# Optimization experiments

Hardware: AMD Instinct MI355X
Metric: run time of the kernel (lower is better)

## Reference

```python
import jax, jax.numpy as jnp
import numpy as np

N = 50000      # num nodes
DIN = 256
DOUT = 256
E = 400000     # edges per sign
NEG_SLOPE = 0.2  # LeakyReLU(0.2)


def setup_inputs() -> dict:
    key = jax.random.key(0)
    ks = jax.random.split(key, 12)
    p = lambda k, shp: jax.random.normal(k, shp, jnp.float32) * 0.05
    return {
        "node_reps": jax.random.normal(ks[0], (N, DIN), jnp.float32),
        "adj_pos": jax.random.randint(ks[1], (2, E), 0, N, dtype=jnp.int32),
        "adj_neg": jax.random.randint(ks[2], (2, E), 0, N, dtype=jnp.int32),
        "basis": p(ks[3], (2, DIN, DOUT)),        # num_bases=num_relations=2
        "att": p(ks[4], (2, 2)),
        "mapping_func": p(ks[5], (1, 2 * DOUT)),
        "bias": p(ks[6], (1, DOUT)),
        "theta1": p(ks[7], (DOUT, DOUT)),          # HGNN_conv 1 linear weight
        "b1": jnp.zeros((DOUT,), jnp.float32),
        "theta2": p(ks[8], (DOUT, DOUT)),          # HGNN_conv 2 linear weight
        "b2": jnp.zeros((DOUT,), jnp.float32),
    }


def reference(node_reps, adj_pos, adj_neg, basis, att, mapping_func, bias,
              theta1, b1, theta2, b2):
    # basis-decomposed relation weights: Wr[r] = sum_b att[r,b] * basis[b]
    Wr = (att @ basis.reshape(2, -1)).reshape(2, DIN, DOUT)
    h_pos = node_reps @ Wr[0]
    h_neg = node_reps @ Wr[1]
    # HGNN_conv feature transforms (linear + bias)
    h_pos = h_pos @ theta1 + b1
    h_neg = h_neg @ theta2 + b2

    # edge attention score: mapping_func . concat(h[src], h[dst])
    w_src = mapping_func[0, :DOUT]
    w_dst = mapping_func[0, DOUT:]
    e_pos = h_pos[adj_pos[0]] @ w_src + h_pos[adj_pos[1]] @ w_dst  # [E]
    e_neg = h_neg[adj_neg[0]] @ w_src + h_neg[adj_neg[1]] @ w_dst  # [E]
    e_all = jnp.concatenate([e_pos, e_neg])                         # [2E]
    coeff = jax.nn.sigmoid(jnp.where(e_all > 0, e_all, NEG_SLOPE * e_all))

    # symmetric degree normalization over the union graph
    rows_all = jnp.concatenate([adj_pos[0], adj_neg[0]])
    cols_all = jnp.concatenate([adj_pos[1], adj_neg[1]])
    deg = jnp.sqrt(jax.ops.segment_sum(
        jnp.ones_like(coeff), rows_all, num_segments=N))            # [N]
    coeff = coeff / (deg[rows_all] * deg[cols_all])

    # sparse aggregation (SpecialSpmm): out[r] += coeff_e * h[c]
    h_agg_pos = jax.ops.segment_sum(
        coeff[:E, None] * h_pos[adj_pos[1]], adj_pos[0], num_segments=N)
    h_agg_neg = jax.ops.segment_sum(
        coeff[E:, None] * h_neg[adj_neg[1]], adj_neg[0], num_segments=N)

    output = h_agg_pos - h_agg_neg + bias
    return (output, h_agg_pos, h_agg_neg)
```

## Files before the change

kernel.cpp:

```cpp
#include <hip/hip_runtime.h>

#define N_NODES 50000
#define NEDGE   400000
#define SB      512
#define NSB     ((N_NODES + SB - 1) / SB)

typedef __bf16 bf16x8 __attribute__((ext_vector_type(8)));
typedef float  f32x4  __attribute__((ext_vector_type(4)));
typedef unsigned short u16x8 __attribute__((ext_vector_type(8)));

#define GLDS16(gp, lp) \
  __builtin_amdgcn_global_load_lds((const __attribute__((address_space(1))) void*)(gp), \
                                   (__attribute__((address_space(3))) void*)(lp), 16, 0, 0)

static __device__ __forceinline__ unsigned short f2bf(float f) {
  unsigned u = __float_as_uint(f);
  unsigned r = (u + 0x7fffu + ((u >> 16) & 1u)) >> 16;
  return (unsigned short)r;
}
static __device__ __forceinline__ float bf2f(unsigned short v) {
  return __uint_as_float((unsigned)v << 16);
}

__global__ void prep_kernel(const float* __restrict__ basis, const float* __restrict__ att,
                            const float* __restrict__ theta1, const float* __restrict__ theta2,
                            const float* __restrict__ bias1, const float* __restrict__ bias2,
                            unsigned short* __restrict__ Wt, float* __restrict__ biasvec) {
  const int bid = blockIdx.x;
  const int r = bid >> 8, k = bid & 255;
  const int n = threadIdx.x;
  const float a0 = att[r * 2 + 0], a1 = att[r * 2 + 1];
  const float* th = (r == 0) ? theta1 : theta2;
  float acc = 0.f;
  for (int j = 0; j < 256; ++j) {
    const float wr = a0 * basis[k * 256 + j] + a1 * basis[65536 + k * 256 + j];
    acc += wr * th[j * 256 + n];
  }
  Wt[(size_t)(r * 256 + n) * 256 + k] = f2bf(acc);
  if (k == 0) biasvec[r * 256 + n] = (r == 0) ? bias1[n] : bias2[n];
}

__global__ void cast_kernel(const float* __restrict__ in, unsigned short* __restrict__ out) {
  const long total = (long)N_NODES * 256 / 4;
  long idx = (long)blockIdx.x * blockDim.x + threadIdx.x;
  const long stride = (long)gridDim.x * blockDim.x;
  for (; idx < total; idx += stride) {
    const f32x4 v = __builtin_nontemporal_load(&((const f32x4*)in)[idx]);
    ushort4 o;
    o.x = f2bf(v.x); o.y = f2bf(v.y); o.z = f2bf(v.z); o.w = f2bf(v.w);
    ((ushort4*)out)[idx] = o;
  }
}

__global__ __launch_bounds__(256) void gemm_kernel(
    const unsigned short* __restrict__ A,
    const unsigned short* __restrict__ Wt,
    const float* __restrict__ biasvec,
    const float* __restrict__ mapping,
    unsigned short* __restrict__ H,
    float* __restrict__ sdbuf) {
  __shared__ unsigned short smem[128 * 136];
  unsigned short* sA = smem;
  unsigned short* sB = smem + 8192;
  const int tid = threadIdx.x;
  const int wave = tid >> 6, lane = tid & 63;
  const int wm = wave >> 1, wn = wave & 1;
  const int m0 = blockIdx.y * 128;
  const int n0 = blockIdx.x * 128;

  f32x4 acc[4][4];
#pragma unroll
  for (int a = 0; a < 4; ++a)
#pragma unroll
    for (int b = 0; b < 4; ++b) acc[a][b] = (f32x4){0.f, 0.f, 0.f, 0.f};

  const int srow = lane >> 3;
  const int skel = ((lane & 7) ^ srow) << 3;

  for (int ks = 0; ks < 4; ++ks) {
    const int kg = ks * 64 + skel;
#pragma unroll
    for (int c = 0; c < 4; ++c) {
      const int chunk = wave * 4 + c;
      const int row = chunk * 8 + srow;
      int rowg = m0 + row;
      rowg = rowg < N_NODES ? rowg : N_NODES - 1;
      GLDS16(A + (size_t)rowg * 256 + kg, sA + chunk * 512);
      GLDS16(Wt + (size_t)(n0 + row) * 256 + kg, sB + chunk * 512);
    }
    __syncthreads();
#pragma unroll
    for (int kk = 0; kk < 2; ++kk) {
      const int kb = (kk * 32 + ((lane >> 4) << 3)) << 1;
      bf16x8 af[4], bfr[4];
#pragma unroll
      for (int m16 = 0; m16 < 4; ++m16) {
        const int row = wm * 64 + m16 * 16 + (lane & 15);
        af[m16] = *(const bf16x8*)((const char*)sA + row * 128 + (kb ^ ((row & 7) << 4)));
      }
#pragma unroll
      for (int n16 = 0; n16 < 4; ++n16) {
        const int col = wn * 64 + n16 * 16 + (lane & 15);
        bfr[n16] = *(const bf16x8*)((const char*)sB + col * 128 + (kb ^ ((col & 7) << 4)));
      }
#pragma unroll
      for (int m16 = 0; m16 < 4; ++m16)
#pragma unroll
        for (int n16 = 0; n16 < 4; ++n16)
          acc[m16][n16] = __builtin_amdgcn_mfma_f32_16x16x32_bf16(af[m16], bfr[n16], acc[m16][n16], 0, 0, 0);
    }
    __syncthreads();
  }

  const bool sgn = (n0 >= 256);
  const int nb = (sgn ? (n0 - 256) : n0) >> 7;
  const int slice = nb * 2 + wn;
  float* __restrict__ sS = sdbuf + ((size_t)((sgn ? 2 : 0) + 0) * 4 + slice) * N_NODES;
  float* __restrict__ sD = sdbuf + ((size_t)((sgn ? 2 : 0) + 1) * 4 + slice) * N_NODES;
  float bv[4], wsv[4], wdv[4];
#pragma unroll
  for (int n16 = 0; n16 < 4; ++n16) {
    const int colg = n0 + wn * 64 + n16 * 16 + (lane & 15);
    bv[n16] = biasvec[colg];
    const int cm = colg & 255;
    wsv[n16] = mapping[cm];
    wdv[n16] = mapping[256 + cm];
  }
#pragma unroll
  for (int m16 = 0; m16 < 4; ++m16) {
    const int rowb = wm * 64 + m16 * 16 + ((lane >> 4) << 2);
#pragma unroll
    for (int j = 0; j < 4; ++j) {
      const int rowl = rowb + j;
      float vs = 0.f, vd = 0.f;
#pragma unroll
      for (int n16 = 0; n16 < 4; ++n16) {
        const float v = acc[m16][n16][j] + bv[n16];
        const int coll = wn * 64 + n16 * 16 + (lane & 15);
        smem[rowl * 136 + coll] = f2bf(v);
        vs += v * wsv[n16];
        vd += v * wdv[n16];
      }
#pragma unroll
      for (int off = 1; off < 16; off <<= 1) { vs += __shfl_xor(vs, off); vd += __shfl_xor(vd, off); }
      const int rowg = m0 + rowl;
      if ((lane & 15) == 0 && rowg < N_NODES) { sS[rowg] = vs; sD[rowg] = vd; }
    }
  }
  __syncthreads();
#pragma unroll
  for (int it = 0; it < 8; ++it) {
    const int row = it * 16 + (tid >> 4);
    const int c8 = (tid & 15) * 8;
    const int rowg = m0 + row;
    if (rowg < N_NODES) {
      const u16x8 v = *(const u16x8*)(smem + row * 136 + c8);
      *(u16x8*)(&H[(size_t)rowg * 512 + n0 + c8]) = v;
    }
  }
}

__global__ void count_kernel(const int* __restrict__ adjp, const int* __restrict__ adjn,
                             int* __restrict__ cntp, int* __restrict__ cntn) {
  const int g = blockIdx.x * blockDim.x + threadIdx.x;
  if (g >= 2 * NEDGE) return;
  if (g < NEDGE) atomicAdd(&cntp[adjp[g]], 1);
  else           atomicAdd(&cntn[adjn[g - NEDGE]], 1);
}

__global__ __launch_bounds__(SB) void scan1_kernel(const int* __restrict__ cntp,
                                                   const int* __restrict__ cntn,
                                                   int* __restrict__ bsp, int* __restrict__ bsn) {
  __shared__ int lp[SB / 64], ln[SB / 64];
  const int i = blockIdx.x * SB + threadIdx.x;
  int vp = (i < N_NODES) ? cntp[i] : 0;
  int vn = (i < N_NODES) ? cntn[i] : 0;
#pragma unroll
  for (int off = 1; off < 64; off <<= 1) { vp += __shfl_xor(vp, off); vn += __shfl_xor(vn, off); }
  const int wave = threadIdx.x >> 6, lane = threadIdx.x & 63;
  if (lane == 0) { lp[wave] = vp; ln[wave] = vn; }
  __syncthreads();
  if (threadIdx.x == 0) {
    int ap = 0, an = 0;
#pragma unroll
    for (int w = 0; w < SB / 64; ++w) { ap += lp[w]; an += ln[w]; }
    bsp[blockIdx.x] = ap; bsn[blockIdx.x] = an;
  }
}

__global__ void scan2_kernel(int* __restrict__ bsp, int* __restrict__ bsn,
                             int* __restrict__ rsp, int* __restrict__ rsn) {
  __shared__ int sp_[128], sn_[128];
  const int t = threadIdx.x;
  sp_[t] = (t < NSB) ? bsp[t] : 0;
  sn_[t] = (t < NSB) ? bsn[t] : 0;
  __syncthreads();
  for (int off = 1; off < 128; off <<= 1) {
    const int ap = (t >= off) ? sp_[t - off] : 0;
    const int an = (t >= off) ? sn_[t - off] : 0;
    __syncthreads();
    sp_[t] += ap; sn_[t] += an;
    __syncthreads();
  }
  if (t < NSB) { bsp[t] = (t == 0) ? 0 : sp_[t - 1]; bsn[t] = (t == 0) ? 0 : sn_[t - 1]; }
  if (t == 127) { rsp[N_NODES] = sp_[127]; rsn[N_NODES] = sn_[127]; }
}

__global__ __launch_bounds__(SB) void scan3_kernel(const int* __restrict__ cntp,
                                                   const int* __restrict__ cntn,
                                                   const int* __restrict__ bsp,
                                                   const int* __restrict__ bsn,
                                                   int* __restrict__ rsp, int* __restrict__ rsn,
                                                   int* __restrict__ curp, int* __restrict__ curn,
                                                   float* __restrict__ rdeg) {
  __shared__ int sp_[SB], sn_[SB];
  const int t = threadIdx.x;
  const int i = blockIdx.x * SB + t;
  const int cp = (i < N_NODES) ? cntp[i] : 0;
  const int cn = (i < N_NODES) ? cntn[i] : 0;
  sp_[t] = cp; sn_[t] = cn;
  __syncthreads();
  for (int off = 1; off < SB; off <<= 1) {
    const int ap = (t >= off) ? sp_[t - off] : 0;
    const int an = (t >= off) ? sn_[t - off] : 0;
    __syncthreads();
    sp_[t] += ap; sn_[t] += an;
    __syncthreads();
  }
  if (i < N_NODES) {
    const int rp = bsp[blockIdx.x] + sp_[t] - cp;
    const int rn = bsn[blockIdx.x] + sn_[t] - cn;
    rsp[i] = rp; curp[i] = rp;
    rsn[i] = rn; curn[i] = rn;
    rdeg[i] = 1.f / sqrtf((float)(cp + cn));
  }
}

__global__ void scatter_kernel(const int* __restrict__ adjp, const int* __restrict__ adjn,
                               const float* __restrict__ sdbuf,
                               const float* __restrict__ rdeg,
                               int* __restrict__ curp, int* __restrict__ curn,
                               int* __restrict__ colp, float* __restrict__ cfp,
                               int* __restrict__ coln, float* __restrict__ cfn) {
  const int g = blockIdx.x * blockDim.x + threadIdx.x;
  if (g >= 2 * NEDGE) return;
  const bool neg = (g >= NEDGE);
  const int e2 = neg ? g - NEDGE : g;
  const int* __restrict__ adj = neg ? adjn : adjp;
  const float* __restrict__ Sb = sdbuf + (size_t)(neg ? 8 : 0) * N_NODES;
  const float* __restrict__ Db = sdbuf + (size_t)(neg ? 12 : 4) * N_NODES;
  int* __restrict__ cur = neg ? curn : curp;
  int* __restrict__ col = neg ? coln : colp;
  float* __restrict__ cf = neg ? cfn : cfp;
  const int src = adj[e2], dst = adj[NEDGE + e2];
  float e = 0.f;
#pragma unroll
  for (int sl = 0; sl < 4; ++sl) e += Sb[(size_t)sl * N_NODES + src] + Db[(size_t)sl * N_NODES + dst];
  const float l = e > 0.f ? e : 0.2f * e;
  const float c = (1.f / (1.f + expf(-l))) * rdeg[src] * rdeg[dst];
  const int p = atomicAdd(&cur[src], 1);
  col[p] = dst; cf[p] = c;
}

__global__ __launch_bounds__(256) void agg_kernel(
    const unsigned short* __restrict__ H,
    const int* __restrict__ rsp, const int* __restrict__ colp, const float* __restrict__ cfp,
    const int* __restrict__ rsn, const int* __restrict__ coln, const float* __restrict__ cfn,
    const float* __restrict__ bias, float* __restrict__ out) {
  __shared__ f32x4 sneg[2][64];
  const int wave = threadIdx.x >> 6, lane = threadIdx.x & 63;
  const int r = wave >> 1;
  const int sign = wave & 1;
  const int i = blockIdx.x * 2 + r;
  const int* __restrict__ rs  = sign ? rsn : rsp;
  const int* __restrict__ col = sign ? coln : colp;
  const float* __restrict__ cf = sign ? cfn : cfp;
  const unsigned short* __restrict__ Hb = H + sign * 256 + (size_t)lane * 4;
  const int beg = rs[i], end = rs[i + 1];
  f32x4 a0 = {0,0,0,0}, a1 = {0,0,0,0}, a2 = {0,0,0,0}, a3 = {0,0,0,0};
  for (int chunk = beg; chunk < end; chunk += 64) {
    const int m = (end - chunk < 64) ? end - chunk : 64;
    const int   cv = (lane < m) ? col[chunk + lane] : 0;
    const float fv = (lane < m) ? cf[chunk + lane] : 0.f;
    int k = 0;
    for (; k + 4 <= m; k += 4) {
      const int   c0 = __shfl(cv, k),     c1 = __shfl(cv, k + 1);
      const int   c2 = __shfl(cv, k + 2), c3 = __shfl(cv, k + 3);
      const float f0 = __shfl(fv, k),     f1 = __shfl(fv, k + 1);
      const float f2 = __shfl(fv, k + 2), f3 = __shfl(fv, k + 3);
      const ushort4 h0 = *(const ushort4*)(Hb + (size_t)c0 * 512);
      const ushort4 h1 = *(const ushort4*)(Hb + (size_t)c1 * 512);
      const ushort4 h2 = *(const ushort4*)(Hb + (size_t)c2 * 512);
      const ushort4 h3 = *(const ushort4*)(Hb + (size_t)c3 * 512);
      a0.x += f0 * bf2f(h0.x); a0.y += f0 * bf2f(h0.y); a0.z += f0 * bf2f(h0.z); a0.w += f0 * bf2f(h0.w);
      a1.x += f1 * bf2f(h1.x); a1.y += f1 * bf2f(h1.y); a1.z += f1 * bf2f(h1.z); a1.w += f1 * bf2f(h1.w);
      a2.x += f2 * bf2f(h2.x); a2.y += f2 * bf2f(h2.y); a2.z += f2 * bf2f(h2.z); a2.w += f2 * bf2f(h2.w);
      a3.x += f3 * bf2f(h3.x); a3.y += f3 * bf2f(h3.y); a3.z += f3 * bf2f(h3.z); a3.w += f3 * bf2f(h3.w);
    }
    for (; k < m; ++k) {
      const int   c0 = __shfl(cv, k);
      const float f0 = __shfl(fv, k);
      const ushort4 h0 = *(const ushort4*)(Hb + (size_t)c0 * 512);
      a0.x += f0 * bf2f(h0.x); a0.y += f0 * bf2f(h0.y); a0.z += f0 * bf2f(h0.z); a0.w += f0 * bf2f(h0.w);
    }
  }
  f32x4 a = (a0 + a1) + (a2 + a3);
  if (sign) sneg[r][lane] = a;
  __syncthreads();
  if (sign) {
    __builtin_nontemporal_store(a, ((f32x4*)(out + (size_t)2 * N_NODES * 256)) + (size_t)i * 64 + lane);
  } else {
    const f32x4 an = sneg[r][lane];
    const f32x4 bv = ((const f32x4*)bias)[lane];
    const f32x4 o = a - an + bv;
    __builtin_nontemporal_store(o, ((f32x4*)out) + (size_t)i * 64 + lane);
    __builtin_nontemporal_store(a, ((f32x4*)(out + (size_t)N_NODES * 256)) + (size_t)i * 64 + lane);
  }
}

extern "C" void kernel_launch(void* const* d_in, const int* in_sizes, int n_in,
                              void* d_out, int out_size, void* d_ws, size_t ws_size,
                              hipStream_t stream) {
  const float* node    = (const float*)d_in[0];
  const int*   adjp    = (const int*)d_in[1];
  const int*   adjn    = (const int*)d_in[2];
  const float* basis   = (const float*)d_in[3];
  const float* att     = (const float*)d_in[4];
  const float* mapping = (const float*)d_in[5];
  const float* bias    = (const float*)d_in[6];
  const float* theta1  = (const float*)d_in[7];
  const float* b1      = (const float*)d_in[8];
  const float* theta2  = (const float*)d_in[9];
  const float* b2      = (const float*)d_in[10];
  float* out = (float*)d_out;

  size_t off = 0;
  char* wsb = (char*)d_ws;
  auto alloc = [&](size_t bytes) -> char* {
    char* p = wsb + off;
    off = (off + bytes + 255) & ~(size_t)255;
    return p;
  };
  unsigned short* A16 = (unsigned short*)alloc((size_t)N_NODES * 256 * 2);
  unsigned short* H   = (unsigned short*)alloc((size_t)N_NODES * 512 * 2);
  unsigned short* Wt  = (unsigned short*)alloc(512 * 256 * 2);
  float* biasvec = (float*)alloc(512 * 4);
  float* sdbuf = (float*)alloc((size_t)16 * N_NODES * 4);
  float* rdeg = (float*)alloc(N_NODES * 4);
  int* cnt2 = (int*)alloc((size_t)2 * N_NODES * 4);
  int* cntp = cnt2, *cntn = cnt2 + N_NODES;
  int* cur2 = (int*)alloc((size_t)2 * N_NODES * 4);
  int* curp = cur2, *curn = cur2 + N_NODES;
  int* rsp = (int*)alloc((N_NODES + 1) * 4);
  int* rsn = (int*)alloc((N_NODES + 1) * 4);
  int* bsp = (int*)alloc(NSB * 4);
  int* bsn = (int*)alloc(NSB * 4);
  int*   colp = (int*)alloc((size_t)NEDGE * 4);
  float* cfp  = (float*)alloc((size_t)NEDGE * 4);
  int*   coln = (int*)alloc((size_t)NEDGE * 4);
  float* cfn  = (float*)alloc((size_t)NEDGE * 4);

  (void)hipMemsetAsync(cnt2, 0, (size_t)2 * N_NODES * 4, stream);

  prep_kernel<<<512, 256, 0, stream>>>(basis, att, theta1, theta2, b1, b2, Wt, biasvec);
  cast_kernel<<<2048, 256, 0, stream>>>(node, A16);
  gemm_kernel<<<dim3(4, 391), 256, 0, stream>>>(A16, Wt, biasvec, mapping, H, sdbuf);
  count_kernel<<<(2 * NEDGE) / 256, 256, 0, stream>>>(adjp, adjn, cntp, cntn);
  scan1_kernel<<<NSB, SB, 0, stream>>>(cntp, cntn, bsp, bsn);
  scan2_kernel<<<1, 128, 0, stream>>>(bsp, bsn, rsp, rsn);
  scan3_kernel<<<NSB, SB, 0, stream>>>(cntp, cntn, bsp, bsn, rsp, rsn, curp, curn, rdeg);
  scatter_kernel<<<(2 * NEDGE) / 256, 256, 0, stream>>>(adjp, adjn, sdbuf, rdeg,
                                                        curp, curn, colp, cfp, coln, cfn);
  agg_kernel<<<N_NODES / 2, 256, 0, stream>>>(H, rsp, colp, cfp, rsn, coln, cfn, bias, out);
}
```

Baseline: 246.9 us.

## Fuse prep/cast/count kernels and pack per-node and per-edge data into vectors

```diff
diff --git a/kernel.cpp b/kernel.cpp
--- a/kernel.cpp
+++ b/kernel.cpp
@@ -8,6 +8,7 @@
 typedef __bf16 bf16x8 __attribute__((ext_vector_type(8)));
 typedef float  f32x4  __attribute__((ext_vector_type(4)));
 typedef unsigned short u16x8 __attribute__((ext_vector_type(8)));
+typedef int    i32x2  __attribute__((ext_vector_type(2)));
 
 #define GLDS16(gp, lp) \
   __builtin_amdgcn_global_load_lds((const __attribute__((address_space(1))) void*)(gp), \
@@ -22,33 +23,41 @@
   return __uint_as_float((unsigned)v << 16);
 }
 
-__global__ void prep_kernel(const float* __restrict__ basis, const float* __restrict__ att,
-                            const float* __restrict__ theta1, const float* __restrict__ theta2,
-                            const float* __restrict__ bias1, const float* __restrict__ bias2,
-                            unsigned short* __restrict__ Wt, float* __restrict__ biasvec) {
-  const int bid = blockIdx.x;
-  const int r = bid >> 8, k = bid & 255;
-  const int n = threadIdx.x;
-  const float a0 = att[r * 2 + 0], a1 = att[r * 2 + 1];
-  const float* th = (r == 0) ? theta1 : theta2;
-  float acc = 0.f;
-  for (int j = 0; j < 256; ++j) {
-    const float wr = a0 * basis[k * 256 + j] + a1 * basis[65536 + k * 256 + j];
-    acc += wr * th[j * 256 + n];
-  }
-  Wt[(size_t)(r * 256 + n) * 256 + k] = f2bf(acc);
-  if (k == 0) biasvec[r * 256 + n] = (r == 0) ? bias1[n] : bias2[n];
-}
-
-__global__ void cast_kernel(const float* __restrict__ in, unsigned short* __restrict__ out) {
-  const long total = (long)N_NODES * 256 / 4;
-  long idx = (long)blockIdx.x * blockDim.x + threadIdx.x;
-  const long stride = (long)gridDim.x * blockDim.x;
-  for (; idx < total; idx += stride) {
-    const f32x4 v = __builtin_nontemporal_load(&((const f32x4*)in)[idx]);
-    ushort4 o;
-    o.x = f2bf(v.x); o.y = f2bf(v.y); o.z = f2bf(v.z); o.w = f2bf(v.w);
-    ((ushort4*)out)[idx] = o;
+__global__ __launch_bounds__(256) void fused0_kernel(
+    const float* __restrict__ basis, const float* __restrict__ att,
+    const float* __restrict__ theta1, const float* __restrict__ theta2,
+    const float* __restrict__ bias1, const float* __restrict__ bias2,
+    unsigned short* __restrict__ Wt, float* __restrict__ biasvec,
+    const float* __restrict__ node, unsigned short* __restrict__ A16,
+    const int* __restrict__ adjp, const int* __restrict__ adjn,
+    int* __restrict__ cntp, int* __restrict__ cntn) {
+  const int b = blockIdx.x;
+  if (b < 512) {
+    const int r = b >> 8, k = b & 255;
+    const int n = threadIdx.x;
+    const float a0 = att[r * 2 + 0], a1 = att[r * 2 + 1];
+    const float* th = (r == 0) ? theta1 : theta2;
+    float acc = 0.f;
+    for (int j = 0; j < 256; ++j) {
+      const float wr = a0 * basis[k * 256 + j] + a1 * basis[65536 + k * 256 + j];
+      acc += wr * th[j * 256 + n];
+    }
+    Wt[(size_t)(r * 256 + n) * 256 + k] = f2bf(acc);
+    if (k == 0) biasvec[r * 256 + n] = (r == 0) ? bias1[n] : bias2[n];
+  } else if (b < 2560) {
+    const long total = (long)N_NODES * 256 / 4;
+    long idx = (long)(b - 512) * 256 + threadIdx.x;
+    const long stride = 2048L * 256;
+    for (; idx < total; idx += stride) {
+      const f32x4 v = __builtin_nontemporal_load(&((const f32x4*)node)[idx]);
+      ushort4 o;
+      o.x = f2bf(v.x); o.y = f2bf(v.y); o.z = f2bf(v.z); o.w = f2bf(v.w);
+      ((ushort4*)A16)[idx] = o;
+    }
+  } else {
+    const int g = (b - 2560) * 256 + threadIdx.x;
+    if (g < NEDGE) atomicAdd(&cntp[adjp[g]], 1);
+    else if (g < 2 * NEDGE) atomicAdd(&cntn[adjn[g - NEDGE]], 1);
   }
 }
 
@@ -160,14 +169,6 @@
   }
 }
 
-__global__ void count_kernel(const int* __restrict__ adjp, const int* __restrict__ adjn,
-                             int* __restrict__ cntp, int* __restrict__ cntn) {
-  const int g = blockIdx.x * blockDim.x + threadIdx.x;
-  if (g >= 2 * NEDGE) return;
-  if (g < NEDGE) atomicAdd(&cntp[adjp[g]], 1);
-  else           atomicAdd(&cntn[adjn[g - NEDGE]], 1);
-}
-
 __global__ __launch_bounds__(SB) void scan1_kernel(const int* __restrict__ cntp,
                                                    const int* __restrict__ cntn,
                                                    int* __restrict__ bsp, int* __restrict__ bsn) {
@@ -210,9 +211,10 @@
                                                    const int* __restrict__ cntn,
                                                    const int* __restrict__ bsp,
                                                    const int* __restrict__ bsn,
+                                                   const float* __restrict__ sdbuf,
                                                    int* __restrict__ rsp, int* __restrict__ rsn,
                                                    int* __restrict__ curp, int* __restrict__ curn,
-                                                   float* __restrict__ rdeg) {
+                                                   f32x4* __restrict__ nip, f32x4* __restrict__ nin) {
   __shared__ int sp_[SB], sn_[SB];
   const int t = threadIdx.x;
   const int i = blockIdx.x * SB + t;
@@ -232,40 +234,46 @@
     const int rn = bsn[blockIdx.x] + sn_[t] - cn;
     rsp[i] = rp; curp[i] = rp;
     rsn[i] = rn; curn[i] = rn;
-    rdeg[i] = 1.f / sqrtf((float)(cp + cn));
+    const float rdeg = 1.f / sqrtf((float)(cp + cn));
+    float sp4 = 0.f, dp4 = 0.f, sn4 = 0.f, dn4 = 0.f;
+#pragma unroll
+    for (int sl = 0; sl < 4; ++sl) {
+      sp4 += sdbuf[(size_t)(0 * 4 + sl) * N_NODES + i];
+      dp4 += sdbuf[(size_t)(1 * 4 + sl) * N_NODES + i];
+      sn4 += sdbuf[(size_t)(2 * 4 + sl) * N_NODES + i];
+      dn4 += sdbuf[(size_t)(3 * 4 + sl) * N_NODES + i];
+    }
+    nip[i] = (f32x4){sp4, dp4, rdeg, 0.f};
+    nin[i] = (f32x4){sn4, dn4, rdeg, 0.f};
   }
 }
 
 __global__ void scatter_kernel(const int* __restrict__ adjp, const int* __restrict__ adjn,
-                               const float* __restrict__ sdbuf,
-                               const float* __restrict__ rdeg,
+                               const f32x4* __restrict__ nip, const f32x4* __restrict__ nin,
                                int* __restrict__ curp, int* __restrict__ curn,
-                               int* __restrict__ colp, float* __restrict__ cfp,
-                               int* __restrict__ coln, float* __restrict__ cfn) {
+                               i32x2* __restrict__ ecp, i32x2* __restrict__ ecn) {
   const int g = blockIdx.x * blockDim.x + threadIdx.x;
   if (g >= 2 * NEDGE) return;
   const bool neg = (g >= NEDGE);
   const int e2 = neg ? g - NEDGE : g;
   const int* __restrict__ adj = neg ? adjn : adjp;
-  const float* __restrict__ Sb = sdbuf + (size_t)(neg ? 8 : 0) * N_NODES;
-  const float* __restrict__ Db = sdbuf + (size_t)(neg ? 12 : 4) * N_NODES;
+  const f32x4* __restrict__ ni = neg ? nin : nip;
   int* __restrict__ cur = neg ? curn : curp;
-  int* __restrict__ col = neg ? coln : colp;
-  float* __restrict__ cf = neg ? cfn : cfp;
+  i32x2* __restrict__ ec = neg ? ecn : ecp;
   const int src = adj[e2], dst = adj[NEDGE + e2];
-  float e = 0.f;
-#pragma unroll
-  for (int sl = 0; sl < 4; ++sl) e += Sb[(size_t)sl * N_NODES + src] + Db[(size_t)sl * N_NODES + dst];
+  const f32x4 a = ni[src], b = ni[dst];
+  const float e = a.x + b.y;
   const float l = e > 0.f ? e : 0.2f * e;
-  const float c = (1.f / (1.f + expf(-l))) * rdeg[src] * rdeg[dst];
+  const float c = (1.f / (1.f + expf(-l))) * a.z * b.z;
   const int p = atomicAdd(&cur[src], 1);
-  col[p] = dst; cf[p] = c;
+  i32x2 w; w.x = dst; w.y = __float_as_int(c);
+  ec[p] = w;
 }
 
 __global__ __launch_bounds__(256) void agg_kernel(
     const unsigned short* __restrict__ H,
-    const int* __restrict__ rsp, const int* __restrict__ colp, const float* __restrict__ cfp,
-    const int* __restrict__ rsn, const int* __restrict__ coln, const float* __restrict__ cfn,
+    const int* __restrict__ rsp, const i32x2* __restrict__ ecp,
+    const int* __restrict__ rsn, const i32x2* __restrict__ ecn,
     const float* __restrict__ bias, float* __restrict__ out) {
   __shared__ f32x4 sneg[2][64];
   const int wave = threadIdx.x >> 6, lane = threadIdx.x & 63;
@@ -273,15 +281,16 @@
   const int sign = wave & 1;
   const int i = blockIdx.x * 2 + r;
   const int* __restrict__ rs  = sign ? rsn : rsp;
-  const int* __restrict__ col = sign ? coln : colp;
-  const float* __restrict__ cf = sign ? cfn : cfp;
+  const i32x2* __restrict__ ec = sign ? ecn : ecp;
   const unsigned short* __restrict__ Hb = H + sign * 256 + (size_t)lane * 4;
   const int beg = rs[i], end = rs[i + 1];
   f32x4 a0 = {0,0,0,0}, a1 = {0,0,0,0}, a2 = {0,0,0,0}, a3 = {0,0,0,0};
   for (int chunk = beg; chunk < end; chunk += 64) {
     const int m = (end - chunk < 64) ? end - chunk : 64;
-    const int   cv = (lane < m) ? col[chunk + lane] : 0;
-    const float fv = (lane < m) ? cf[chunk + lane] : 0.f;
+    i32x2 ev = {0, 0};
+    if (lane < m) ev = __builtin_nontemporal_load(&ec[chunk + lane]);
+    const int   cv = ev.x;
+    const float fv = __int_as_float(ev.y);
     int k = 0;
     for (; k + 4 <= m; k += 4) {
       const int   c0 = __shfl(cv, k),     c1 = __shfl(cv, k + 1);
@@ -346,7 +355,8 @@
   unsigned short* Wt  = (unsigned short*)alloc(512 * 256 * 2);
   float* biasvec = (float*)alloc(512 * 4);
   float* sdbuf = (float*)alloc((size_t)16 * N_NODES * 4);
-  float* rdeg = (float*)alloc(N_NODES * 4);
+  f32x4* nip = (f32x4*)alloc((size_t)N_NODES * 16);
+  f32x4* nin = (f32x4*)alloc((size_t)N_NODES * 16);
   int* cnt2 = (int*)alloc((size_t)2 * N_NODES * 4);
   int* cntp = cnt2, *cntn = cnt2 + N_NODES;
   int* cur2 = (int*)alloc((size_t)2 * N_NODES * 4);
@@ -355,21 +365,17 @@
   int* rsn = (int*)alloc((N_NODES + 1) * 4);
   int* bsp = (int*)alloc(NSB * 4);
   int* bsn = (int*)alloc(NSB * 4);
-  int*   colp = (int*)alloc((size_t)NEDGE * 4);
-  float* cfp  = (float*)alloc((size_t)NEDGE * 4);
-  int*   coln = (int*)alloc((size_t)NEDGE * 4);
-  float* cfn  = (float*)alloc((size_t)NEDGE * 4);
+  i32x2* ecp = (i32x2*)alloc((size_t)NEDGE * 8);
+  i32x2* ecn = (i32x2*)alloc((size_t)NEDGE * 8);
 
   (void)hipMemsetAsync(cnt2, 0, (size_t)2 * N_NODES * 4, stream);
 
-  prep_kernel<<<512, 256, 0, stream>>>(basis, att, theta1, theta2, b1, b2, Wt, biasvec);
-  cast_kernel<<<2048, 256, 0, stream>>>(node, A16);
+  fused0_kernel<<<512 + 2048 + (2 * NEDGE) / 256, 256, 0, stream>>>(
+      basis, att, theta1, theta2, b1, b2, Wt, biasvec, node, A16, adjp, adjn, cntp, cntn);
   gemm_kernel<<<dim3(4, 391), 256, 0, stream>>>(A16, Wt, biasvec, mapping, H, sdbuf);
-  count_kernel<<<(2 * NEDGE) / 256, 256, 0, stream>>>(adjp, adjn, cntp, cntn);
   scan1_kernel<<<NSB, SB, 0, stream>>>(cntp, cntn, bsp, bsn);
   scan2_kernel<<<1, 128, 0, stream>>>(bsp, bsn, rsp, rsn);
-  scan3_kernel<<<NSB, SB, 0, stream>>>(cntp, cntn, bsp, bsn, rsp, rsn, curp, curn, rdeg);
-  scatter_kernel<<<(2 * NEDGE) / 256, 256, 0, stream>>>(adjp, adjn, sdbuf, rdeg,
-                                                        curp, curn, colp, cfp, coln, cfn);
-  agg_kernel<<<N_NODES / 2, 256, 0, stream>>>(H, rsp, colp, cfp, rsn, coln, cfn, bias, out);
-}
+  scan3_kernel<<<NSB, SB, 0, stream>>>(cntp, cntn, bsp, bsn, sdbuf, rsp, rsn, curp, curn, nip, nin);
+  scatter_kernel<<<(2 * NEDGE) / 256, 256, 0, stream>>>(adjp, adjn, nip, nin, curp, curn, ecp, ecn);
+  agg_kernel<<<N_NODES / 2, 256, 0, stream>>>(H, rsp, ecp, rsn, ecn, bias, out);
+}
```

Result: faster. 227.4 us (-7.9%).
